# Kernel optimization log

Measured on AMD Instinct MI355X. Metric: run time of the kernel, lower is better.

Reference implementation:

```python
import jax, jax.numpy as jnp
import numpy as np
from jax import lax

B, N, S, K = 16, 4096, 1024, 32  # batch, points, sampled points (npoint), neighbors (nsample)
D_IN = 64                        # point feature channels
MLP = [64, 64, 128]
EPS = 1e-5


def setup_inputs() -> dict:
    key = jax.random.key(0)
    ks = jax.random.split(key, 16)
    inp = {
        "xyz": jax.random.normal(ks[0], (B, 3, N), jnp.float32),
        "points": jax.random.normal(ks[1], (B, D_IN, N), jnp.float32),
    }
    last = D_IN + 3  # first_layer=False -> concat grouped_xyz_norm (3 dims)
    for i, out in enumerate(MLP, start=1):
        inp[f"W{i}"] = jax.random.normal(ks[1 + 3 * i], (out, last), jnp.float32) * (1.0 / np.sqrt(last))
        inp[f"b{i}"] = jnp.zeros((out,), jnp.float32)
        inp[f"g{i}"] = jnp.ones((out,), jnp.float32)
        inp[f"be{i}"] = jnp.zeros((out,), jnp.float32)
        last = out
    return inp


def _fps(xyz):
    # xyz: [B, N, 3] -> indices [B, S] via farthest point sampling (start at idx 0)
    b, n, _ = xyz.shape
    batch_ar = jnp.arange(b)

    def step(carry, _):
        dist, farthest = carry          # dist [B,N], farthest [B]
        centroid = xyz[batch_ar, farthest]            # [B,3]
        d = jnp.sum((xyz - centroid[:, None, :]) ** 2, axis=-1)
        dist = jnp.minimum(dist, d)
        return (dist, jnp.argmax(dist, axis=-1)), farthest

    init = (jnp.full((b, n), 1e10, xyz.dtype), jnp.zeros((b,), jnp.int32))
    _, idxs = lax.scan(step, init, None, length=S)  # [S, B]
    return idxs.T  # [B, S]


def _bn_relu(x, g, b):
    # train-mode BatchNorm2d over axes (0,2,3), biased variance, then ReLU
    m = jnp.mean(x, axis=(0, 2, 3), keepdims=True)
    v = jnp.mean((x - m) ** 2, axis=(0, 2, 3), keepdims=True)
    xn = (x - m) * lax.rsqrt(v + EPS)
    return jax.nn.relu(g[None, :, None, None] * xn + b[None, :, None, None])


def reference(xyz, points, W1, b1, g1, be1, W2, b2, g2, be2, W3, b3, g3, be3):
    xyz_n = jnp.transpose(xyz, (0, 2, 1))      # [B,N,3]
    pts_n = jnp.transpose(points, (0, 2, 1))   # [B,N,D]

    fps_idx = _fps(xyz_n)                                       # [B,S]
    new_xyz = jnp.take_along_axis(xyz_n, fps_idx[:, :, None], axis=1)  # [B,S,3]

    # squared pairwise distances [B,S,N], then kNN via argsort (matches torch argsort[:K])
    sq_s = jnp.sum(new_xyz ** 2, axis=-1)                       # [B,S]
    sq_n = jnp.sum(xyz_n ** 2, axis=-1)                         # [B,N]
    dist = sq_s[:, :, None] + sq_n[:, None, :] - 2.0 * jnp.einsum("bsc,bnc->bsn", new_xyz, xyz_n)
    idx = jnp.argsort(dist, axis=-1)[:, :, :K]                  # [B,S,K]

    grouped_xyz = jnp.take_along_axis(xyz_n[:, None, :, :], idx[..., None], axis=2)  # [B,S,K,3]
    grouped_xyz_norm = grouped_xyz - new_xyz[:, :, None, :]
    grouped_pts = jnp.take_along_axis(pts_n[:, None, :, :], idx[..., None], axis=2)  # [B,S,K,D]
    g = jnp.concatenate([grouped_pts, grouped_xyz_norm], axis=-1)  # [B,S,K,D+3]
    g = jnp.transpose(g, (0, 3, 2, 1))                             # [B,C,K,S]

    for W, b, gm, bt in ((W1, b1, g1, be1), (W2, b2, g2, be2), (W3, b3, g3, be3)):
        g = jnp.einsum("oc,bcks->boks", W, g) + b[None, :, None, None]
        g = _bn_relu(g, gm, bt)

    new_points = jnp.max(g, axis=2)                 # [B, 128, S]
    return jnp.transpose(new_xyz, (0, 2, 1)), new_points
```

## Files before the change

kernel.cpp:

```cpp
#include <hip/hip_runtime.h>
#include <hip/hip_bf16.h>


typedef __attribute__((ext_vector_type(8))) short bfrag;
typedef __attribute__((ext_vector_type(4))) float ffrag;
typedef __attribute__((ext_vector_type(8))) unsigned short ushort8;

#define XS 104

__device__ inline unsigned short f2bf(float f){
  union { float f; unsigned u; } v; v.f = f;
  unsigned r = v.u + 0x7fffu + ((v.u >> 16) & 1u);
  return (unsigned short)(r >> 16);
}
__device__ inline float bf2f(unsigned short h){
  union { unsigned u; float f; } v; v.u = ((unsigned)h) << 16; return v.f;
}

template<int CTRL> __device__ __forceinline__ int dppi(int v){
  return __builtin_amdgcn_update_dpp(0, v, CTRL, 0xF, 0xF, true);
}
template<int CTRL> __device__ __forceinline__ float dppf(float v){
  return __int_as_float(dppi<CTRL>(__float_as_int(v)));
}
__device__ __forceinline__ float dppmax6(float v){
  v = fmaxf(v, dppf<0xB1>(v)); v = fmaxf(v, dppf<0x4E>(v));
  v = fmaxf(v, dppf<0x141>(v)); v = fmaxf(v, dppf<0x140>(v));
  v = fmaxf(v, dppf<0x142>(v)); v = fmaxf(v, dppf<0x143>(v));
  return v;
}
__device__ __forceinline__ float dppmin6(float v){
  v = fminf(v, dppf<0xB1>(v)); v = fminf(v, dppf<0x4E>(v));
  v = fminf(v, dppf<0x141>(v)); v = fminf(v, dppf<0x140>(v));
  v = fminf(v, dppf<0x142>(v)); v = fminf(v, dppf<0x143>(v));
  return v;
}
__device__ __forceinline__ unsigned dppminu6(unsigned v){
  unsigned o;
  o = (unsigned)dppi<0xB1>((int)v);  v = v < o ? v : o;
  o = (unsigned)dppi<0x4E>((int)v);  v = v < o ? v : o;
  o = (unsigned)dppi<0x141>((int)v); v = v < o ? v : o;
  o = (unsigned)dppi<0x140>((int)v); v = v < o ? v : o;
  o = (unsigned)dppi<0x142>((int)v); v = v < o ? v : o;
  o = (unsigned)dppi<0x143>((int)v); v = v < o ? v : o;
  return v;
}
__device__ __forceinline__ float dppadd4(float v){
  v += dppf<0xB1>(v); v += dppf<0x4E>(v); v += dppf<0x141>(v); v += dppf<0x140>(v);
  return v;
}
__device__ __forceinline__ float dppmax4(float v){
  v = fmaxf(v, dppf<0xB1>(v)); v = fmaxf(v, dppf<0x4E>(v));
  v = fmaxf(v, dppf<0x141>(v)); v = fmaxf(v, dppf<0x140>(v));
  return v;
}
__device__ __forceinline__ float dppmin4(float v){
  v = fminf(v, dppf<0xB1>(v)); v = fminf(v, dppf<0x4E>(v));
  v = fminf(v, dppf<0x141>(v)); v = fminf(v, dppf<0x140>(v));
  return v;
}

__global__ __launch_bounds__(256) void wconv_k(const float* __restrict__ W1,
    const float* __restrict__ W2, const float* __restrict__ W3,
    unsigned short* __restrict__ Wb1, unsigned short* __restrict__ Wb2,
    unsigned short* __restrict__ Wb3, float* __restrict__ stats, int* __restrict__ farr){
  const int t = threadIdx.x;
  for (int i = t; i < 64 * 96; i += 256){
    int r = i / 96, c = i % 96;
    Wb1[i] = (c < 67) ? f2bf(W1[r * 67 + c]) : (unsigned short)0;
  }
  for (int i = t; i < 64 * 64; i += 256) Wb2[i] = f2bf(W2[i]);
  for (int i = t; i < 128 * 64; i += 256) Wb3[i] = f2bf(W3[i]);
  for (int i = t; i < 32768; i += 256) stats[i] = 0.f;
  for (int i = t; i < 16384; i += 256) farr[i] = 0;
}

__global__ __launch_bounds__(512) void fused_k(const float* __restrict__ xyz,
    const float* __restrict__ pts, unsigned short* __restrict__ pts_t, float* __restrict__ xyz_t,
    float* __restrict__ out0, float* __restrict__ new_xyz,
    int* __restrict__ farr, int* __restrict__ knn){
  __shared__ __align__(16) char smem[98304];
  const int t = threadIdx.x, bid = blockIdx.x;
  if (bid >= 272){
    const int bid2 = bid - 272;
    const int w = t >> 6, lane = t & 63;
    const int b = bid2 & 15;
    const int s = (bid2 >> 4) * 8 + w;
    const float* xb = xyz + (size_t)b * 3 * 4096;
    int fidx;
    while ((fidx = atomicAdd(&farr[b * 1024 + s], 0)) == 0)
      __builtin_amdgcn_s_sleep(16);
    const int far = fidx - 1;
    const float cx = xb[far], cy = xb[4096 + far], cz = xb[8192 + far];
    const float sqc = __fadd_rn(__fadd_rn(__fmul_rn(cx, cx), __fmul_rn(cy, cy)), __fmul_rn(cz, cz));
    float d[64];
    float m1 = 3e38f, m2 = 3e38f, m3 = 3e38f, m4 = 3e38f;
    int i1 = 0x7fffffff, i2 = 0x7fffffff, i3 = 0x7fffffff, i4 = 0x7fffffff;
    #pragma unroll
    for (int j = 0; j < 64; j++){
      int i = j * 64 + lane;
      float x = xb[i], y = xb[4096 + i], z = xb[8192 + i];
      float sqn = __fadd_rn(__fadd_rn(__fmul_rn(x, x), __fmul_rn(y, y)), __fmul_rn(z, z));
      float dot = __fadd_rn(__fadd_rn(__fmul_rn(cx, x), __fmul_rn(cy, y)), __fmul_rn(cz, z));
      float dd = __fsub_rn(__fadd_rn(sqc, sqn), __fmul_rn(2.0f, dot));
      d[j] = dd;
      bool c1 = dd < m1, c2 = dd < m2, c3 = dd < m3, c4 = dd < m4;
      m4 = c4 ? (c3 ? m3 : dd) : m4;  i4 = c4 ? (c3 ? i3 : i) : i4;
      m3 = c3 ? (c2 ? m2 : dd) : m3;  i3 = c3 ? (c2 ? i2 : i) : i3;
      m2 = c2 ? (c1 ? m1 : dd) : m2;  i2 = c2 ? (c1 ? i1 : i) : i2;
      m1 = c1 ? dd : m1;              i1 = c1 ? i : i1;
    }
    unsigned long long taken = 0ull;
    int out_idx = 0;
    #pragma unroll 1
    for (int r = 0; r < 32; r++){
      const float gred = dppmin6(m1);
      const float gmin = __int_as_float(__builtin_amdgcn_readlane(__float_as_int(gred), 63));
      const bool cand = (m1 == gmin);
      const unsigned long long cm = __ballot(cand);
      int widx;
      if (__popcll(cm) == 1){
        widx = __builtin_amdgcn_readlane(i1, (int)(__ffsll(cm) - 1));
      } else {
        unsigned ci = cand ? (unsigned)i1 : 0xFFFFFFFFu;
        widx = (int)__builtin_amdgcn_readlane((int)dppminu6(ci), 63);
      }
      if (lane == r) out_idx = widx;
      if (i1 == widx){
        taken |= 1ull << (widx >> 6);
        m1 = m2; i1 = i2; m2 = m3; i2 = i3; m3 = m4; i3 = i4;
        m4 = 3e38f; i4 = 0x7fffffff;
        if (i1 == 0x7fffffff){
          m1 = 3e38f; m2 = 3e38f; m3 = 3e38f; m4 = 3e38f;
          i1 = 0x7fffffff; i2 = 0x7fffffff; i3 = 0x7fffffff; i4 = 0x7fffffff;
          #pragma unroll
          for (int j = 0; j < 64; j++){
            if (!((taken >> j) & 1ull)){
              float dd = d[j]; int i = j * 64 + lane;
              bool c1 = dd < m1, c2 = dd < m2, c3 = dd < m3, c4 = dd < m4;
              m4 = c4 ? (c3 ? m3 : dd) : m4;  i4 = c4 ? (c3 ? i3 : i) : i4;
              m3 = c3 ? (c2 ? m2 : dd) : m3;  i3 = c3 ? (c2 ? i2 : i) : i3;
              m2 = c2 ? (c1 ? m1 : dd) : m2;  i2 = c2 ? (c1 ? i1 : i) : i2;
              m1 = c1 ? dd : m1;              i1 = c1 ? i : i1;
            }
          }
        }
      }
    }
    if (lane < 32) knn[((size_t)(b * 1024 + s)) * 32 + lane] = out_idx;
    return;
  }
  if (bid >= 16){
    unsigned short* tile = (unsigned short*)smem;
    const int bid2 = bid - 16;
    const int b = bid2 >> 4, n0 = (bid2 & 15) * 256;
    {
      const int n = t & 255, ch = t >> 8;
      for (int it = 0; it < 32; it++){
        int c = it * 2 + ch;
        tile[c * 258 + n] = f2bf(pts[((size_t)(b * 64 + c)) * 4096 + n0 + n]);
      }
    }
    __syncthreads();
    const int nn = t >> 5, c2 = (t & 31) * 2;
    for (int rep = 0; rep < 16; rep++){
      int n = rep * 16 + nn;
      unsigned lo = tile[c2 * 258 + n], hi = tile[(c2 + 1) * 258 + n];
      ((unsigned*)pts_t)[(((size_t)(b * 4096 + n0 + n)) * 64 + c2) >> 1] = lo | (hi << 16);
    }
    if (t < 256){
      float x = xyz[((size_t)(b * 3 + 0)) * 4096 + n0 + t];
      float y = xyz[((size_t)(b * 3 + 1)) * 4096 + n0 + t];
      float z = xyz[((size_t)(b * 3 + 2)) * 4096 + n0 + t];
      float* dst = &xyz_t[((size_t)(b * 4096 + n0 + t)) * 3];
      dst[0] = x; dst[1] = y; dst[2] = z;
    }
    return;
  }
  float4* xl4 = (float4*)smem;
  unsigned long long* skey = (unsigned long long*)(smem + 65536);
  unsigned short* farhist = (unsigned short*)(smem + 65568);
  const int b = bid;
  {
    const float* xb = xyz + (size_t)b * 3 * 4096;
    for (int j = 0; j < 8; j++){
      int i = j * 512 + t;
      float4 v; v.x = xb[i]; v.y = xb[4096 + i]; v.z = xb[8192 + i]; v.w = 0.f;
      xl4[i] = v;
    }
  }
  if (t == 0){
    skey[0] = 0xFFFFFFFF00000FFFull;
    skey[1] = 0ull; skey[2] = 0ull; skey[3] = 0ull;
  }
  __syncthreads();
  float px[8], py[8], pz[8], dist[8];
  #pragma unroll
  for (int j = 0; j < 8; j++){
    int i = j * 512 + t;
    float4 v = xl4[i];
    px[j] = v.x; py[j] = v.y; pz[j] = v.z; dist[j] = 1e10f;
  }
  const unsigned a0 = 4095u - t;
  for (int s = 0; s < 1024; s++){
    const unsigned long long kg = skey[s & 3];
    const int far = 4095 - (int)(unsigned)(kg & 0xFFFFFFFFull);
    const float4 c4 = xl4[far];
    const float cx = c4.x, cy = c4.y, cz = c4.z;
    if (t == 0){
      farhist[s] = (unsigned short)far;
      skey[(s + 2) & 3] = 0ull;
      atomicExch(&farr[b * 1024 + s], far + 1);
    }
    float vm = -1.f;
    #pragma unroll
    for (int j = 0; j < 8; j++){
      float dx = __fsub_rn(px[j], cx), dy = __fsub_rn(py[j], cy), dz = __fsub_rn(pz[j], cz);
      float d = __fadd_rn(__fadd_rn(__fmul_rn(dx, dx), __fmul_rn(dy, dy)), __fmul_rn(dz, dz));
      float dm = fminf(dist[j], d); dist[j] = dm;
      vm = fmaxf(vm, dm);
    }
    const float wred = dppmax6(vm);
    const float wvm = __int_as_float(__builtin_amdgcn_readlane(__float_as_int(wred), 63));
    if (vm == wvm){
      unsigned inv = 0u;
      #pragma unroll
      for (int j = 7; j >= 0; j--)
        if (dist[j] == wvm) inv = a0 - (unsigned)(j * 512);
      atomicMax(&skey[(s + 1) & 3],
                (((unsigned long long)__float_as_uint(wvm)) << 32) | inv);
    }
    __syncthreads();
  }
  for (int s2 = t; s2 < 1024; s2 += 512){
    const int f = farhist[s2];
    const float4 c4 = xl4[f];
    out0[(b * 3 + 0) * 1024 + s2] = c4.x;
    out0[(b * 3 + 1) * 1024 + s2] = c4.y;
    out0[(b * 3 + 2) * 1024 + s2] = c4.z;
    float* nx = &new_xyz[(b * 1024 + s2) * 3];
    nx[0] = c4.x; nx[1] = c4.y; nx[2] = c4.z;
  }
}


__global__ __launch_bounds__(256) void gemm1_k(const unsigned short* __restrict__ pts_t,
    const float* __restrict__ xyz_t, const float* __restrict__ new_xyz,
    const int* __restrict__ knn, const unsigned short* __restrict__ Wb1, const float* __restrict__ b1,
    unsigned short* __restrict__ z1, float* __restrict__ stats){
  __shared__ unsigned short Xl[256 * XS];
  __shared__ float bsum[128];
  const int t = threadIdx.x, bid = blockIdx.x;
  const int b = bid >> 7, col0 = (bid & 127) * 256;
  if (t < 128) bsum[t] = 0.f;
  {
    const int col = col0 + t, s = col >> 5, k = col & 31;
    const int idx = knn[((size_t)(b * 1024 + s)) * 32 + k];
    const unsigned short* src = pts_t + ((size_t)(b * 4096 + idx)) * 64;
    #pragma unroll
    for (int j = 0; j < 8; j++) *(ushort8*)&Xl[t * XS + j * 8] = *(const ushort8*)&src[j * 8];
    const float* nx = &new_xyz[(b * 1024 + s) * 3];
    const float* gx = &xyz_t[((size_t)(b * 4096 + idx)) * 3];
    ushort8 tail = {0,0,0,0,0,0,0,0};
    tail[0] = f2bf(__fsub_rn(gx[0], nx[0]));
    tail[1] = f2bf(__fsub_rn(gx[1], nx[1]));
    tail[2] = f2bf(__fsub_rn(gx[2], nx[2]));
    *(ushort8*)&Xl[t * XS + 64] = tail;
    ushort8 zz8 = {0,0,0,0,0,0,0,0};
    *(ushort8*)&Xl[t * XS + 72] = zz8;
    *(ushort8*)&Xl[t * XS + 80] = zz8;
    *(ushort8*)&Xl[t * XS + 88] = zz8;
  }
  const int lane = t & 63, lr = lane & 15, lg = lane >> 4;
  const int colw = (t >> 6) * 64;
  bfrag a[4][3];
  #pragma unroll
  for (int r = 0; r < 4; r++)
    #pragma unroll
    for (int kk = 0; kk < 3; kk++)
      a[r][kk] = *(const bfrag*)&Wb1[(16 * r + lr) * 96 + kk * 32 + lg * 8];
  __syncthreads();
  ffrag acc[4][4] = {};
  #pragma unroll
  for (int kk = 0; kk < 3; kk++){
    bfrag bb[4];
    #pragma unroll
    for (int cf = 0; cf < 4; cf++)
      bb[cf] = *(const bfrag*)&Xl[(colw + cf * 16 + lr) * XS + kk * 32 + lg * 8];
    #pragma unroll
    for (int r = 0; r < 4; r++)
      #pragma unroll
      for (int cf = 0; cf < 4; cf++)
        acc[r][cf] = __builtin_amdgcn_mfma_f32_16x16x32_bf16(a[r][kk], bb[cf], acc[r][cf], 0, 0, 0);
  }
  #pragma unroll
  for (int r = 0; r < 4; r++){
    const int o0 = 16 * r + 4 * lg;
    const ffrag bv = *(const ffrag*)&b1[o0];
    float sm[4] = {0,0,0,0}, sq[4] = {0,0,0,0};
    #pragma unroll
    for (int cf = 0; cf < 4; cf++){
      const int col = col0 + colw + cf * 16 + lr;
      unsigned pk[2];
      #pragma unroll
      for (int e = 0; e < 4; e++){
        float v = acc[r][cf][e] + bv[e];
        sm[e] += v; sq[e] += v * v;
        ((unsigned short*)pk)[e] = f2bf(v);
      }
      *(unsigned long long*)&z1[((size_t)(b * 32768) + col) * 64 + o0] = *(unsigned long long*)pk;
    }
    #pragma unroll
    for (int e = 0; e < 4; e++){
      float s1 = dppadd4(sm[e]);
      float q1 = dppadd4(sq[e]);
      if (lr == 0){ atomicAdd(&bsum[(o0 + e) * 2], s1); atomicAdd(&bsum[(o0 + e) * 2 + 1], q1); }
    }
  }
  __syncthreads();
  if (t < 128) atomicAdd(&stats[(bid & 63) * 128 + t], bsum[t]);
}

__global__ __launch_bounds__(256) void gemm2_k(const unsigned short* __restrict__ z1,
    const unsigned short* __restrict__ Wb2, const float* __restrict__ b2, const float* __restrict__ p1,
    unsigned short* __restrict__ z2, float* __restrict__ stats){
  __shared__ unsigned short Xl[256 * XS];
  __shared__ float bsum[128];
  __shared__ float pa[64], pc[64];
  const int t = threadIdx.x, bid = blockIdx.x;
  const int b = bid >> 7, col0 = (bid & 127) * 256;
  if (t < 128) bsum[t] = 0.f;
  if (t < 64){ pa[t] = p1[t * 2]; pc[t] = p1[t * 2 + 1]; }
  const int lane = t & 63, lr = lane & 15, lg = lane >> 4;
  const int colw = (t >> 6) * 64;
  bfrag a[4][2];
  #pragma unroll
  for (int r = 0; r < 4; r++)
    #pragma unroll
    for (int kk = 0; kk < 2; kk++)
      a[r][kk] = *(const bfrag*)&Wb2[(16 * r + lr) * 64 + kk * 32 + lg * 8];
  __syncthreads();
  {
    const size_t gcol = (size_t)b * 32768 + col0 + t;
    const unsigned short* src = z1 + gcol * 64;
    #pragma unroll
    for (int j = 0; j < 8; j++){
      ushort8 zv = *(const ushort8*)&src[j * 8];
      unsigned short ov[8];
      #pragma unroll
      for (int e = 0; e < 8; e++){
        int ch = j * 8 + e;
        float v = fmaxf(fmaf(pa[ch], bf2f(zv[e]), pc[ch]), 0.f);
        ov[e] = f2bf(v);
      }
      *(ushort8*)&Xl[t * XS + j * 8] = *(ushort8*)ov;
    }
  }
  __syncthreads();
  ffrag acc[4][4] = {};
  #pragma unroll
  for (int kk = 0; kk < 2; kk++){
    bfrag bb[4];
    #pragma unroll
    for (int cf = 0; cf < 4; cf++)
      bb[cf] = *(const bfrag*)&Xl[(colw + cf * 16 + lr) * XS + kk * 32 + lg * 8];
    #pragma unroll
    for (int r = 0; r < 4; r++)
      #pragma unroll
      for (int cf = 0; cf < 4; cf++)
        acc[r][cf] = __builtin_amdgcn_mfma_f32_16x16x32_bf16(a[r][kk], bb[cf], acc[r][cf], 0, 0, 0);
  }
  #pragma unroll
  for (int r = 0; r < 4; r++){
    const int o0 = 16 * r + 4 * lg;
    const ffrag bv = *(const ffrag*)&b2[o0];
    float sm[4] = {0,0,0,0}, sq[4] = {0,0,0,0};
    #pragma unroll
    for (int cf = 0; cf < 4; cf++){
      const int col = col0 + colw + cf * 16 + lr;
      unsigned pk[2];
      #pragma unroll
      for (int e = 0; e < 4; e++){
        float v = acc[r][cf][e] + bv[e];
        sm[e] += v; sq[e] += v * v;
        ((unsigned short*)pk)[e] = f2bf(v);
      }
      *(unsigned long long*)&z2[((size_t)(b * 32768) + col) * 64 + o0] = *(unsigned long long*)pk;
    }
    #pragma unroll
    for (int e = 0; e < 4; e++){
      float s1 = dppadd4(sm[e]);
      float q1 = dppadd4(sq[e]);
      if (lr == 0){ atomicAdd(&bsum[(o0 + e) * 2], s1); atomicAdd(&bsum[(o0 + e) * 2 + 1], q1); }
    }
  }
  __syncthreads();
  if (t < 128) atomicAdd(&stats[(bid & 63) * 128 + t], bsum[t]);
}

__global__ __launch_bounds__(256) void gemm3_k(const unsigned short* __restrict__ z2,
    const unsigned short* __restrict__ Wb3, const float* __restrict__ b3, const float* __restrict__ p2,
    float* __restrict__ maxz, float* __restrict__ minz, float* __restrict__ stats){
  __shared__ unsigned short Xl[128 * XS];
  __shared__ float bsum[256];
  __shared__ float pa[64], pc[64];
  const int t = threadIdx.x, bid = blockIdx.x;
  const int b = bid >> 8, col0 = (bid & 255) * 128;
  bsum[t] = 0.f;
  if (t < 64){ pa[t] = p2[t * 2]; pc[t] = p2[t * 2 + 1]; }
  const int lane = t & 63, lr = lane & 15, lg = lane >> 4;
  const int w = t >> 6, wr = w >> 1, wc = w & 1;
  bfrag a[4][2];
  #pragma unroll
  for (int r = 0; r < 4; r++)
    #pragma unroll
    for (int kk = 0; kk < 2; kk++)
      a[r][kk] = *(const bfrag*)&Wb3[(wr * 64 + 16 * r + lr) * 64 + kk * 32 + lg * 8];
  __syncthreads();
  {
    const int colL = t & 127, half = t >> 7;
    const size_t gcol = (size_t)b * 32768 + col0 + colL;
    const unsigned short* src = z2 + gcol * 64 + half * 32;
    #pragma unroll
    for (int j = 0; j < 4; j++){
      ushort8 zv = *(const ushort8*)&src[j * 8];
      unsigned short ov[8];
      #pragma unroll
      for (int e = 0; e < 8; e++){
        int ch = half * 32 + j * 8 + e;
        float v = fmaxf(fmaf(pa[ch], bf2f(zv[e]), pc[ch]), 0.f);
        ov[e] = f2bf(v);
      }
      *(ushort8*)&Xl[colL * XS + half * 32 + j * 8] = *(ushort8*)ov;
    }
  }
  __syncthreads();
  ffrag acc[4][4] = {};
  #pragma unroll
  for (int kk = 0; kk < 2; kk++){
    bfrag bb[4];
    #pragma unroll
    for (int cf = 0; cf < 4; cf++)
      bb[cf] = *(const bfrag*)&Xl[(wc * 64 + cf * 16 + lr) * XS + kk * 32 + lg * 8];
    #pragma unroll
    for (int r = 0; r < 4; r++)
      #pragma unroll
      for (int cf = 0; cf < 4; cf++)
        acc[r][cf] = __builtin_amdgcn_mfma_f32_16x16x32_bf16(a[r][kk], bb[cf], acc[r][cf], 0, 0, 0);
  }
  const int s0 = (col0 + wc * 64) >> 5;
  #pragma unroll
  for (int r = 0; r < 4; r++){
    const int o0 = wr * 64 + 16 * r + 4 * lg;
    const ffrag bv = *(const ffrag*)&b3[(o0 & 127)];
    float vv[4][4];
    float sm[4] = {0,0,0,0}, sq[4] = {0,0,0,0};
    #pragma unroll
    for (int cf = 0; cf < 4; cf++)
      #pragma unroll
      for (int e = 0; e < 4; e++){
        float v = acc[r][cf][e] + bv[e];
        vv[cf][e] = v; sm[e] += v; sq[e] += v * v;
      }
    #pragma unroll
    for (int e = 0; e < 4; e++){
      float s1 = dppadd4(sm[e]);
      float q1 = dppadd4(sq[e]);
      if (lr == 0){ atomicAdd(&bsum[((o0 + e) & 127) * 2], s1); atomicAdd(&bsum[((o0 + e) & 127) * 2 + 1], q1); }
    }
    #pragma unroll
    for (int si = 0; si < 2; si++){
      ffrag mx, mn;
      #pragma unroll
      for (int e = 0; e < 4; e++){
        mx[e] = dppmax4(fmaxf(vv[si * 2][e], vv[si * 2 + 1][e]));
        mn[e] = dppmin4(fminf(vv[si * 2][e], vv[si * 2 + 1][e]));
      }
      if (lr == 0){
        *(ffrag*)&maxz[((size_t)(b * 1024) + s0 + si) * 128 + o0] = mx;
        *(ffrag*)&minz[((size_t)(b * 1024) + s0 + si) * 128 + o0] = mn;
      }
    }
  }
  __syncthreads();
  atomicAdd(&stats[(bid & 63) * 256 + t], bsum[t]);
}

template<int CH>
__global__ void stats_k(const float* __restrict__ stats, const float* __restrict__ gamma,
                        const float* __restrict__ beta, float* __restrict__ params){
  const int t = threadIdx.x;
  float sm = 0.f, sq = 0.f;
  for (int sl = 0; sl < 64; sl++){
    sm += stats[sl * (CH * 2) + t * 2];
    sq += stats[sl * (CH * 2) + t * 2 + 1];
  }
  const float cnt = 524288.f;
  float mean = sm / cnt;
  float var = sq / cnt - mean * mean;
  if (var < 0.f) var = 0.f;
  float inv = gamma[t] / sqrtf(var + 1e-5f);
  params[t * 2] = inv;
  params[t * 2 + 1] = beta[t] - mean * inv;
}

__global__ __launch_bounds__(256) void final_k(const float* __restrict__ maxz,
    const float* __restrict__ minz, const float* __restrict__ p3, float* __restrict__ out1){
  __shared__ float tile[64][129];
  __shared__ float pa[128], pc[128];
  const int t = threadIdx.x, bid = blockIdx.x;
  const int b = bid >> 4, s0 = (bid & 15) * 64;
  if (t < 128){ pa[t] = p3[t * 2]; pc[t] = p3[t * 2 + 1]; }
  __syncthreads();
  const int o = t & 127, rr = t >> 7;
  for (int it = 0; it < 32; it++){
    int srow = it * 2 + rr;
    size_t base = ((size_t)(b * 1024) + s0 + srow) * 128 + o;
    float aa = pa[o], cc = pc[o];
    float m = (aa >= 0.f) ? maxz[base] : minz[base];
    tile[srow][o] = fmaxf(fmaf(aa, m, cc), 0.f);
  }
  __syncthreads();
  const int sc = t & 63, og = t >> 6;
  for (int it = 0; it < 32; it++){
    int o2 = it * 4 + og;
    out1[((size_t)(b * 128 + o2)) * 1024 + s0 + sc] = tile[sc][o2];
  }
}

extern "C" void kernel_launch(void* const* d_in, const int* in_sizes, int n_in,
                              void* d_out, int out_size, void* d_ws, size_t ws_size,
                              hipStream_t stream){
  const float* xyz = (const float*)d_in[0];
  const float* pts = (const float*)d_in[1];
  const float* W1 = (const float*)d_in[2];  const float* b1 = (const float*)d_in[3];
  const float* g1 = (const float*)d_in[4];  const float* be1 = (const float*)d_in[5];
  const float* W2 = (const float*)d_in[6];  const float* b2 = (const float*)d_in[7];
  const float* g2 = (const float*)d_in[8];  const float* be2 = (const float*)d_in[9];
  const float* W3 = (const float*)d_in[10]; const float* b3 = (const float*)d_in[11];
  const float* g3 = (const float*)d_in[12]; const float* be3 = (const float*)d_in[13];
  float* out0 = (float*)d_out;
  float* out1 = out0 + 16 * 3 * 1024;

  char* w = (char*)d_ws;
  size_t off = 0;
  auto alloc = [&](size_t bytes){ void* p = w + off; off = (off + bytes + 255) & ~(size_t)255; return p; };
  unsigned short* pts_t = (unsigned short*)alloc(8388608);
  float* xyz_t          = (float*)alloc(786432);
  float* new_xyz        = (float*)alloc(196608);
  int*   knn            = (int*)alloc(2097152);
  unsigned short* z1    = (unsigned short*)alloc(67108864);
  unsigned short* z2    = (unsigned short*)alloc(67108864);
  float* maxz           = (float*)alloc(8388608);
  float* minz           = (float*)alloc(8388608);
  unsigned short* Wb1   = (unsigned short*)alloc(12288);
  unsigned short* Wb2   = (unsigned short*)alloc(8192);
  unsigned short* Wb3   = (unsigned short*)alloc(16384);
  float* stats          = (float*)alloc(131072);
  float* params         = (float*)alloc(2048);
  int*   farr           = (int*)alloc(65536);
  if (ws_size < off) return;

  float* stats1 = stats;
  float* stats2 = stats + 8192;
  float* stats3 = stats + 16384;
  float* p1 = params, *p2 = params + 128, *p3 = params + 256;

  wconv_k<<<1, 256, 0, stream>>>(W1, W2, W3, Wb1, Wb2, Wb3, stats, farr);
  fused_k<<<2320, 512, 0, stream>>>(xyz, pts, pts_t, xyz_t, out0, new_xyz, farr, knn);
  gemm1_k<<<2048, 256, 0, stream>>>(pts_t, xyz_t, new_xyz, knn, Wb1, b1, z1, stats1);
  stats_k<64><<<1, 64, 0, stream>>>(stats1, g1, be1, p1);
  gemm2_k<<<2048, 256, 0, stream>>>(z1, Wb2, b2, p1, z2, stats2);
  stats_k<64><<<1, 64, 0, stream>>>(stats2, g2, be2, p2);
  gemm3_k<<<4096, 256, 0, stream>>>(z2, Wb3, b3, p2, maxz, minz, stats3);
  stats_k<128><<<1, 128, 0, stream>>>(stats3, g3, be3, p3);
  final_k<<<256, 256, 0, stream>>>(maxz, minz, p3, out1);
}
```

Measured before the change: 750.8 us.

## Fuse first-layer gather GEMM into the FPS/kNN kernel with flag-based dataflow

Folds the separate gemm1 kernel into the persistent fused kernel as 1024 extra blocks. Each of these waits on per-centroid kNN done flags and on a transpose completion counter, then gathers neighbours and runs the first MFMA layer. The goal is to overlap layer-1 work with the long serial FPS tail and to drop the xyz_t/new_xyz intermediates by reading the original xyz directly. It also replaces the atomicAdd polling with acquire/release atomic loads and stores. The risk is that blocks spin while waiting, which could hold compute units or deadlock if the dependent blocks are not scheduled before the waiting ones; LDS use per block also grows.

```diff
diff --git a/kernel.cpp b/kernel.cpp
--- a/kernel.cpp
+++ b/kernel.cpp
@@ -63,7 +63,8 @@
 __global__ __launch_bounds__(256) void wconv_k(const float* __restrict__ W1,
     const float* __restrict__ W2, const float* __restrict__ W3,
     unsigned short* __restrict__ Wb1, unsigned short* __restrict__ Wb2,
-    unsigned short* __restrict__ Wb3, float* __restrict__ stats, int* __restrict__ farr){
+    unsigned short* __restrict__ Wb3, float* __restrict__ stats,
+    int* __restrict__ farr, int* __restrict__ kdone, int* __restrict__ tdone){
   const int t = threadIdx.x;
   for (int i = t; i < 64 * 96; i += 256){
     int r = i / 96, c = i % 96;
@@ -72,15 +73,107 @@
   for (int i = t; i < 64 * 64; i += 256) Wb2[i] = f2bf(W2[i]);
   for (int i = t; i < 128 * 64; i += 256) Wb3[i] = f2bf(W3[i]);
   for (int i = t; i < 32768; i += 256) stats[i] = 0.f;
-  for (int i = t; i < 16384; i += 256) farr[i] = 0;
+  for (int i = t; i < 16384; i += 256){ farr[i] = 0; kdone[i] = 0; }
+  if (t == 0) tdone[0] = 0;
 }
 
 __global__ __launch_bounds__(512) void fused_k(const float* __restrict__ xyz,
-    const float* __restrict__ pts, unsigned short* __restrict__ pts_t, float* __restrict__ xyz_t,
-    float* __restrict__ out0, float* __restrict__ new_xyz,
-    int* __restrict__ farr, int* __restrict__ knn){
-  __shared__ __align__(16) char smem[98304];
+    const float* __restrict__ pts, unsigned short* __restrict__ pts_t,
+    float* __restrict__ out0,
+    int* __restrict__ farr, int* __restrict__ kdone, int* __restrict__ tdone,
+    int* __restrict__ knn,
+    const unsigned short* __restrict__ Wb1, const float* __restrict__ b1,
+    unsigned short* __restrict__ z1, float* __restrict__ stats1){
+  __shared__ __align__(16) char smem[107520];
   const int t = threadIdx.x, bid = blockIdx.x;
+  if (bid >= 2320){
+    const int bid2 = bid - 2320;
+    const int sg = bid2 >> 4, b = bid2 & 15;
+    const int col0 = sg * 512;
+    unsigned short* Xl = (unsigned short*)smem;
+    float* bsum = (float*)(smem + 106496);
+    if (t < 128) bsum[t] = 0.f;
+    if (t < 16){
+      while (__hip_atomic_load(&kdone[b * 1024 + sg * 16 + t], __ATOMIC_ACQUIRE,
+                               __HIP_MEMORY_SCOPE_AGENT) == 0)
+        __builtin_amdgcn_s_sleep(16);
+    }
+    if (t == 16){
+      while (__hip_atomic_load(tdone, __ATOMIC_ACQUIRE, __HIP_MEMORY_SCOPE_AGENT) < 256)
+        __builtin_amdgcn_s_sleep(16);
+    }
+    __syncthreads();
+    __threadfence();
+    {
+      const int col = col0 + t, s = col >> 5, k = col & 31;
+      const int idx = __hip_atomic_load(&knn[((size_t)(b * 1024 + s)) * 32 + k],
+                                        __ATOMIC_RELAXED, __HIP_MEMORY_SCOPE_AGENT);
+      const int far = __hip_atomic_load(&farr[b * 1024 + s],
+                                        __ATOMIC_RELAXED, __HIP_MEMORY_SCOPE_AGENT) - 1;
+      const float* xb = xyz + (size_t)b * 3 * 4096;
+      const unsigned short* src = pts_t + ((size_t)(b * 4096 + idx)) * 64;
+      #pragma unroll
+      for (int j = 0; j < 8; j++) *(ushort8*)&Xl[t * XS + j * 8] = *(const ushort8*)&src[j * 8];
+      ushort8 tail = {0,0,0,0,0,0,0,0};
+      tail[0] = f2bf(__fsub_rn(xb[idx],        xb[far]));
+      tail[1] = f2bf(__fsub_rn(xb[4096 + idx], xb[4096 + far]));
+      tail[2] = f2bf(__fsub_rn(xb[8192 + idx], xb[8192 + far]));
+      *(ushort8*)&Xl[t * XS + 64] = tail;
+      ushort8 zz8 = {0,0,0,0,0,0,0,0};
+      *(ushort8*)&Xl[t * XS + 72] = zz8;
+      *(ushort8*)&Xl[t * XS + 80] = zz8;
+      *(ushort8*)&Xl[t * XS + 88] = zz8;
+    }
+    const int lane = t & 63, lr = lane & 15, lg = lane >> 4;
+    const int colw = (t >> 6) * 64;
+    bfrag a[4][3];
+    #pragma unroll
+    for (int r = 0; r < 4; r++)
+      #pragma unroll
+      for (int kk = 0; kk < 3; kk++)
+        a[r][kk] = *(const bfrag*)&Wb1[(16 * r + lr) * 96 + kk * 32 + lg * 8];
+    __syncthreads();
+    ffrag acc[4][4] = {};
+    #pragma unroll
+    for (int kk = 0; kk < 3; kk++){
+      bfrag bb[4];
+      #pragma unroll
+      for (int cf = 0; cf < 4; cf++)
+        bb[cf] = *(const bfrag*)&Xl[(colw + cf * 16 + lr) * XS + kk * 32 + lg * 8];
+      #pragma unroll
+      for (int r = 0; r < 4; r++)
+        #pragma unroll
+        for (int cf = 0; cf < 4; cf++)
+          acc[r][cf] = __builtin_amdgcn_mfma_f32_16x16x32_bf16(a[r][kk], bb[cf], acc[r][cf], 0, 0, 0);
+    }
+    #pragma unroll
+    for (int r = 0; r < 4; r++){
+      const int o0 = 16 * r + 4 * lg;
+      const ffrag bv = *(const ffrag*)&b1[o0];
+      float sm[4] = {0,0,0,0}, sq[4] = {0,0,0,0};
+      #pragma unroll
+      for (int cf = 0; cf < 4; cf++){
+        const int col = col0 + colw + cf * 16 + lr;
+        unsigned pk[2];
+        #pragma unroll
+        for (int e = 0; e < 4; e++){
+          float v = acc[r][cf][e] + bv[e];
+          sm[e] += v; sq[e] += v * v;
+          ((unsigned short*)pk)[e] = f2bf(v);
+        }
+        *(unsigned long long*)&z1[((size_t)(b * 32768) + col) * 64 + o0] = *(unsigned long long*)pk;
+      }
+      #pragma unroll
+      for (int e = 0; e < 4; e++){
+        float s1 = dppadd4(sm[e]);
+        float q1 = dppadd4(sq[e]);
+        if (lr == 0){ atomicAdd(&bsum[(o0 + e) * 2], s1); atomicAdd(&bsum[(o0 + e) * 2 + 1], q1); }
+      }
+    }
+    __syncthreads();
+    if (t < 128) atomicAdd(&stats1[sg * 128 + t], bsum[t]);
+    return;
+  }
   if (bid >= 272){
     const int bid2 = bid - 272;
     const int w = t >> 6, lane = t & 63;
@@ -88,7 +181,8 @@
     const int s = (bid2 >> 4) * 8 + w;
     const float* xb = xyz + (size_t)b * 3 * 4096;
     int fidx;
-    while ((fidx = atomicAdd(&farr[b * 1024 + s], 0)) == 0)
+    while ((fidx = __hip_atomic_load(&farr[b * 1024 + s], __ATOMIC_ACQUIRE,
+                                     __HIP_MEMORY_SCOPE_AGENT)) == 0)
       __builtin_amdgcn_s_sleep(16);
     const int far = fidx - 1;
     const float cx = xb[far], cy = xb[4096 + far], cz = xb[8192 + far];
@@ -147,7 +241,12 @@
         }
       }
     }
-    if (lane < 32) knn[((size_t)(b * 1024 + s)) * 32 + lane] = out_idx;
+    if (lane < 32)
+      __hip_atomic_store(&knn[((size_t)(b * 1024 + s)) * 32 + lane], out_idx,
+                         __ATOMIC_RELAXED, __HIP_MEMORY_SCOPE_AGENT);
+    __threadfence();
+    if (lane == 0)
+      __hip_atomic_store(&kdone[b * 1024 + s], 1, __ATOMIC_RELEASE, __HIP_MEMORY_SCOPE_AGENT);
     return;
   }
   if (bid >= 16){
@@ -168,12 +267,10 @@
       unsigned lo = tile[c2 * 258 + n], hi = tile[(c2 + 1) * 258 + n];
       ((unsigned*)pts_t)[(((size_t)(b * 4096 + n0 + n)) * 64 + c2) >> 1] = lo | (hi << 16);
     }
-    if (t < 256){
-      float x = xyz[((size_t)(b * 3 + 0)) * 4096 + n0 + t];
-      float y = xyz[((size_t)(b * 3 + 1)) * 4096 + n0 + t];
-      float z = xyz[((size_t)(b * 3 + 2)) * 4096 + n0 + t];
-      float* dst = &xyz_t[((size_t)(b * 4096 + n0 + t)) * 3];
-      dst[0] = x; dst[1] = y; dst[2] = z;
+    __syncthreads();
+    if (t == 0){
+      __threadfence();
+      atomicAdd(tdone, 1);
     }
     return;
   }
@@ -210,7 +307,8 @@
     if (t == 0){
       farhist[s] = (unsigned short)far;
       skey[(s + 2) & 3] = 0ull;
-      atomicExch(&farr[b * 1024 + s], far + 1);
+      __hip_atomic_store(&farr[b * 1024 + s], far + 1,
+                         __ATOMIC_RELEASE, __HIP_MEMORY_SCOPE_AGENT);
     }
     float vm = -1.f;
     #pragma unroll
@@ -238,87 +336,7 @@
     out0[(b * 3 + 0) * 1024 + s2] = c4.x;
     out0[(b * 3 + 1) * 1024 + s2] = c4.y;
     out0[(b * 3 + 2) * 1024 + s2] = c4.z;
-    float* nx = &new_xyz[(b * 1024 + s2) * 3];
-    nx[0] = c4.x; nx[1] = c4.y; nx[2] = c4.z;
-  }
-}
-
-
-__global__ __launch_bounds__(256) void gemm1_k(const unsigned short* __restrict__ pts_t,
-    const float* __restrict__ xyz_t, const float* __restrict__ new_xyz,
-    const int* __restrict__ knn, const unsigned short* __restrict__ Wb1, const float* __restrict__ b1,
-    unsigned short* __restrict__ z1, float* __restrict__ stats){
-  __shared__ unsigned short Xl[256 * XS];
-  __shared__ float bsum[128];
-  const int t = threadIdx.x, bid = blockIdx.x;
-  const int b = bid >> 7, col0 = (bid & 127) * 256;
-  if (t < 128) bsum[t] = 0.f;
-  {
-    const int col = col0 + t, s = col >> 5, k = col & 31;
-    const int idx = knn[((size_t)(b * 1024 + s)) * 32 + k];
-    const unsigned short* src = pts_t + ((size_t)(b * 4096 + idx)) * 64;
-    #pragma unroll
-    for (int j = 0; j < 8; j++) *(ushort8*)&Xl[t * XS + j * 8] = *(const ushort8*)&src[j * 8];
-    const float* nx = &new_xyz[(b * 1024 + s) * 3];
-    const float* gx = &xyz_t[((size_t)(b * 4096 + idx)) * 3];
-    ushort8 tail = {0,0,0,0,0,0,0,0};
-    tail[0] = f2bf(__fsub_rn(gx[0], nx[0]));
-    tail[1] = f2bf(__fsub_rn(gx[1], nx[1]));
-    tail[2] = f2bf(__fsub_rn(gx[2], nx[2]));
-    *(ushort8*)&Xl[t * XS + 64] = tail;
-    ushort8 zz8 = {0,0,0,0,0,0,0,0};
-    *(ushort8*)&Xl[t * XS + 72] = zz8;
-    *(ushort8*)&Xl[t * XS + 80] = zz8;
-    *(ushort8*)&Xl[t * XS + 88] = zz8;
-  }
-  const int lane = t & 63, lr = lane & 15, lg = lane >> 4;
-  const int colw = (t >> 6) * 64;
-  bfrag a[4][3];
-  #pragma unroll
-  for (int r = 0; r < 4; r++)
-    #pragma unroll
-    for (int kk = 0; kk < 3; kk++)
-      a[r][kk] = *(const bfrag*)&Wb1[(16 * r + lr) * 96 + kk * 32 + lg * 8];
-  __syncthreads();
-  ffrag acc[4][4] = {};
-  #pragma unroll
-  for (int kk = 0; kk < 3; kk++){
-    bfrag bb[4];
-    #pragma unroll
-    for (int cf = 0; cf < 4; cf++)
-      bb[cf] = *(const bfrag*)&Xl[(colw + cf * 16 + lr) * XS + kk * 32 + lg * 8];
-    #pragma unroll
-    for (int r = 0; r < 4; r++)
-      #pragma unroll
-      for (int cf = 0; cf < 4; cf++)
-        acc[r][cf] = __builtin_amdgcn_mfma_f32_16x16x32_bf16(a[r][kk], bb[cf], acc[r][cf], 0, 0, 0);
-  }
-  #pragma unroll
-  for (int r = 0; r < 4; r++){
-    const int o0 = 16 * r + 4 * lg;
-    const ffrag bv = *(const ffrag*)&b1[o0];
-    float sm[4] = {0,0,0,0}, sq[4] = {0,0,0,0};
-    #pragma unroll
-    for (int cf = 0; cf < 4; cf++){
-      const int col = col0 + colw + cf * 16 + lr;
-      unsigned pk[2];
-      #pragma unroll
-      for (int e = 0; e < 4; e++){
-        float v = acc[r][cf][e] + bv[e];
-        sm[e] += v; sq[e] += v * v;
-        ((unsigned short*)pk)[e] = f2bf(v);
-      }
-      *(unsigned long long*)&z1[((size_t)(b * 32768) + col) * 64 + o0] = *(unsigned long long*)pk;
-    }
-    #pragma unroll
-    for (int e = 0; e < 4; e++){
-      float s1 = dppadd4(sm[e]);
-      float q1 = dppadd4(sq[e]);
-      if (lr == 0){ atomicAdd(&bsum[(o0 + e) * 2], s1); atomicAdd(&bsum[(o0 + e) * 2 + 1], q1); }
-    }
-  }
-  __syncthreads();
-  if (t < 128) atomicAdd(&stats[(bid & 63) * 128 + t], bsum[t]);
+  }
 }
 
 __global__ __launch_bounds__(256) void gemm2_k(const unsigned short* __restrict__ z1,
@@ -546,8 +564,6 @@
   size_t off = 0;
   auto alloc = [&](size_t bytes){ void* p = w + off; off = (off + bytes + 255) & ~(size_t)255; return p; };
   unsigned short* pts_t = (unsigned short*)alloc(8388608);
-  float* xyz_t          = (float*)alloc(786432);
-  float* new_xyz        = (float*)alloc(196608);
   int*   knn            = (int*)alloc(2097152);
   unsigned short* z1    = (unsigned short*)alloc(67108864);
   unsigned short* z2    = (unsigned short*)alloc(67108864);
@@ -559,6 +575,8 @@
   float* stats          = (float*)alloc(131072);
   float* params         = (float*)alloc(2048);
   int*   farr           = (int*)alloc(65536);
+  int*   kdone          = (int*)alloc(65536);
+  int*   tdone          = (int*)alloc(256);
   if (ws_size < off) return;
 
   float* stats1 = stats;
@@ -566,9 +584,9 @@
   float* stats3 = stats + 16384;
   float* p1 = params, *p2 = params + 128, *p3 = params + 256;
 
-  wconv_k<<<1, 256, 0, stream>>>(W1, W2, W3, Wb1, Wb2, Wb3, stats, farr);
-  fused_k<<<2320, 512, 0, stream>>>(xyz, pts, pts_t, xyz_t, out0, new_xyz, farr, knn);
-  gemm1_k<<<2048, 256, 0, stream>>>(pts_t, xyz_t, new_xyz, knn, Wb1, b1, z1, stats1);
+  wconv_k<<<1, 256, 0, stream>>>(W1, W2, W3, Wb1, Wb2, Wb3, stats, farr, kdone, tdone);
+  fused_k<<<3344, 512, 0, stream>>>(xyz, pts, pts_t, out0, farr, kdone, tdone, knn,
+                                    Wb1, b1, z1, stats1);
   stats_k<64><<<1, 64, 0, stream>>>(stats1, g1, be1, p1);
   gemm2_k<<<2048, 256, 0, stream>>>(z1, Wb2, b2, p1, z2, stats2);
   stats_k<64><<<1, 64, 0, stream>>>(stats2, g2, be2, p2);
```

New measurement: 2.107 ms. 2.81x slower.
